# Kernel optimization log

Measured on AMD Instinct MI355X. Metric: run time of the kernel, lower is better.

Reference implementation:

```python
import jax, jax.numpy as jnp
import numpy as np

# Fixed Grossberg constants (registered buffers in the torch module)
TAU = 0.8          # time constant
DECAY = 0.15       # passive decay A
B_CAP = 1.0        # excitatory cap B
C_FLOOR = 0.1      # inhibitory floor C
LAT_INHIB = 3.0    # lateral inhibition strength
DIV_SIGMA = 0.3    # divisive normalization sigma
ALPHA = 1.5        # excitatory gating alpha
BETA = 0.75        # inhibitory gating beta

BATCH = 32768
N = 17
T = 128
DT = 0.05


def _dynamics(state, W_pos, W_neg, feasibility, P):
    """Grossberg shunting ODE right-hand side. state: [B,17]."""
    # valences evaluated with environmental perturbation
    val_eval = state[:, 13:17] + P[:, 13:17]                       # [B,4]
    gate_exc = jax.nn.sigmoid(ALPHA * val_eval)                    # [B,4]
    gate_inh = jax.nn.sigmoid(-BETA * val_eval)                    # [B,4]
    ones9 = jnp.ones_like(state[:, :9])
    ones4 = jnp.ones_like(gate_exc)
    # gates expanded over nodes: only action nodes (9:13) gated
    ge_full = jnp.concatenate([ones9, gate_exc, ones4], axis=1)    # [B,17]
    gi_full = jnp.concatenate([ones9, gate_inh, ones4], axis=1)    # [B,17]
    # row-gating of W is equivalent to gating the matvec output
    exc = ge_full * jnp.einsum('bij,bj->bi', W_pos, state)         # [B,17]
    inh = gi_full * jnp.einsum('bij,bj->bi', W_neg, state)         # [B,17]
    E = jax.nn.relu(exc)
    I = jax.nn.relu(inh)
    # environmental drive routed through shunting terms for need nodes
    E_needs = E[:, :9] + jax.nn.relu(P[:, :9])
    I_needs = I[:, :9] + jax.nn.relu(-P[:, :9])
    # feasibility gates action excitation; selective lateral inhibition:
    # each action inhibited by the (divisively normalized) sum of OTHER actions
    acts = state[:, 9:13]
    other_sum = jnp.sum(acts, axis=1, keepdims=True) - acts
    lateral = LAT_INHIB * other_sum / (DIV_SIGMA + other_sum)
    E_acts = E[:, 9:13] * feasibility
    I_acts = I[:, 9:13] + lateral
    E_full = jnp.concatenate([E_needs, E_acts, E[:, 13:17]], axis=1)
    I_full = jnp.concatenate([I_needs, I_acts, I[:, 13:17]], axis=1)
    # direct additive perturbation only on valence nodes
    P_direct = jnp.concatenate([jnp.zeros_like(state[:, :13]), P[:, 13:17]], axis=1)
    return (-DECAY * state + (B_CAP - state) * E_full
            - (C_FLOOR + state) * I_full + P_direct) / TAU


def setup_inputs() -> dict:
    key = jax.random.key(0)
    k0, k1, k2, k3, k4 = jax.random.split(key, 5)
    state0 = jax.random.uniform(k0, (BATCH, N), dtype=jnp.float32)
    W_pos = 0.2 * jax.random.uniform(k1, (BATCH, N, N), dtype=jnp.float32)
    W_neg = 0.2 * jax.random.uniform(k2, (BATCH, N, N), dtype=jnp.float32)
    feasibility = jax.random.uniform(k3, (BATCH, 4), dtype=jnp.float32)
    perturbation = 0.1 * jax.random.normal(k4, (BATCH, N), dtype=jnp.float32)
    t_eval = jnp.arange(T, dtype=jnp.float32) * DT
    return {"state0": state0, "W_pos": W_pos, "W_neg": W_neg,
            "feasibility": feasibility, "perturbation": perturbation,
            "t_eval": t_eval}


def reference(state0, W_pos, W_neg, feasibility, perturbation, t_eval):
    dt = t_eval[1] - t_eval[0]
    n_steps = t_eval.shape[0] - 1  # static

    def step(s, _):
        ds = _dynamics(s, W_pos, W_neg, feasibility, perturbation)
        raw = s + dt * ds
        new = jnp.concatenate([
            jnp.clip(raw[:, 0:9], 0.0, 1.0),     # needs
            jnp.clip(raw[:, 9:13], 0.0, 1.0),    # actions
            jnp.clip(raw[:, 13:17], -1.0, 1.0),  # valences
        ], axis=1)
        return new, new

    _, traj = jax.lax.scan(step, state0, None, length=n_steps)
    return jnp.concatenate([state0[None], traj], axis=0)  # [T, B, 17]
```

## Files before the change

### kernel.cpp

```cpp
#include <hip/hip_runtime.h>
#include <stdint.h>


typedef _Float16 h2 __attribute__((ext_vector_type(2)));
typedef __fp16 h2raw __attribute__((ext_vector_type(2)));

static constexpr int BATCH = 32768;
static constexpr int NN = 17;
static constexpr int TT = 128;

__device__ __forceinline__ uint32_t pk(float a, float b) {
    h2raw h = __builtin_amdgcn_cvt_pkrtz(a, b);
    return __builtin_bit_cast(uint32_t, h);
}

__device__ __forceinline__ float dot2(uint32_t a, uint32_t b, float c) {
#if __has_builtin(__builtin_amdgcn_fdot2)
    return __builtin_amdgcn_fdot2(__builtin_bit_cast(h2, a),
                                  __builtin_bit_cast(h2, b), c, false);
#else
    h2 ah = __builtin_bit_cast(h2, a), bh = __builtin_bit_cast(h2, b);
    return c + (float)ah.x * (float)bh.x + (float)ah.y * (float)bh.y;
#endif
}

__global__ __launch_bounds__(256, 2) void hotco_kernel(
    const float* __restrict__ state0,
    const float* __restrict__ Wpos,
    const float* __restrict__ Wneg,
    const float* __restrict__ feas,
    const float* __restrict__ P,
    const float* __restrict__ t_eval,
    float* __restrict__ out)
{
    const int tid = blockIdx.x * blockDim.x + threadIdx.x;
    const int lane4 = tid & 3;
    const int b = tid >> 2;
    if (b >= BATCH) return;

    const int base = (lane4 == 0) ? 0 : (4 * lane4 + 1);
    const int nrows = (lane4 == 0) ? 5 : 4;

    constexpr int pA[9] = {0, 2, 4, 5, 7, 9, 11, 13, 15};
    constexpr int pB[9] = {1, 3, -1, 6, 8, 10, 12, 14, 16};

    uint32_t wp[5][9], wn[5][9];
    {
        const float* wpb = Wpos + (size_t)b * (NN * NN);
        const float* wnb = Wneg + (size_t)b * (NN * NN);
#pragma unroll
        for (int t = 0; t < 5; ++t) {
            if (t < nrows) {
                const float* rp = wpb + (base + t) * NN;
                const float* rn = wnb + (base + t) * NN;
#pragma unroll
                for (int c = 0; c < 9; ++c) {
                    float a2 = (pB[c] < 0) ? 0.f : rp[pB[c]];
                    float b2 = (pB[c] < 0) ? 0.f : rn[pB[c]];
                    wp[t][c] = pk(rp[pA[c]], a2);
                    wn[t][c] = pk(rn[pA[c]], b2);
                }
            } else {
#pragma unroll
                for (int c = 0; c < 9; ++c) { wp[t][c] = 0u; wn[t][c] = 0u; }
            }
        }
    }

    uint32_t s2[9];
    {
        float st[17];
#pragma unroll
        for (int j = 0; j < NN; ++j) st[j] = state0[(size_t)b * NN + j];
#pragma unroll
        for (int c = 0; c < 9; ++c)
            s2[c] = pk(st[pA[c]], (pB[c] < 0) ? 0.f : st[pB[c]]);
    }
    float sOwn[5];
#pragma unroll
    for (int t = 0; t < 5; ++t)
        sOwn[t] = (t < nrows) ? state0[(size_t)b * NN + base + t] : 0.f;

    float aE[5], aI[5], pdv[5];
    float gP[4], gF[4];
#pragma unroll
    for (int t = 0; t < 5; ++t) { aE[t] = 0.f; aI[t] = 0.f; pdv[t] = 0.f; }
#pragma unroll
    for (int t = 0; t < 4; ++t) { gP[t] = 0.f; gF[t] = 0.f; }
    if (lane4 < 2) {
#pragma unroll
        for (int t = 0; t < 5; ++t) {
            if (t < nrows) {
                float pv = P[(size_t)b * NN + base + t];
                aE[t] = fmaxf(pv, 0.f);
                aI[t] = fmaxf(-pv, 0.f);
            }
        }
    } else if (lane4 == 2) {
#pragma unroll
        for (int t = 0; t < 4; ++t) {
            gP[t] = P[(size_t)b * NN + 13 + t];
            gF[t] = feas[(size_t)b * 4 + t];
        }
    } else {
#pragma unroll
        for (int t = 0; t < 4; ++t)
            pdv[t] = P[(size_t)b * NN + 13 + t];
    }

    const float lo = (lane4 == 3) ? -1.f : 0.f;
    const float dt = t_eval[1] - t_eval[0];
    const float k1 = dt / 0.8f;
    const float C  = -1.0820212806667226f;

    {
        float* op = out + (size_t)b * NN + base;
#pragma unroll
        for (int t = 0; t < 5; ++t)
            if (t < nrows) op[t] = sOwn[t];
    }
    float* outp = out + (size_t)BATCH * NN + (size_t)b * NN + base;

#pragma unroll 1
    for (int st = 1; st < TT; ++st) {
        float E5[5], I5[5];
#pragma unroll
        for (int t = 0; t < 5; ++t) {
            float ae = 0.f, ai = 0.f;
#pragma unroll
            for (int c = 0; c < 9; ++c) {
                ae = dot2(wp[t][c], s2[c], ae);
                ai = dot2(wn[t][c], s2[c], ai);
            }
            E5[t] = fmaxf(ae, 0.f);
            I5[t] = fmaxf(ai, 0.f);
        }

        if (lane4 == 2) {
            const float sum_acts = sOwn[0] + sOwn[1] + sOwn[2] + sOwn[3];
            h2 q7 = __builtin_bit_cast(h2, s2[7]);
            h2 q8 = __builtin_bit_cast(h2, s2[8]);
            float v13[4] = { (float)q7.x, (float)q7.y, (float)q8.x, (float)q8.y };
#pragma unroll
            for (int t = 0; t < 4; ++t) {
                float v  = v13[t] + gP[t];
                float e1 = __builtin_amdgcn_exp2f(C * v);
                float ge = __builtin_amdgcn_rcpf(fmaf(e1, e1, 1.f));
                float gi = e1 * __builtin_amdgcn_rcpf(1.f + e1);
                E5[t] = ge * E5[t] * gF[t];
                float os  = sum_acts - sOwn[t];
                float lat = fmaf(-0.9f, __builtin_amdgcn_rcpf(0.3f + os), 3.0f);
                I5[t] = fmaf(gi, I5[t], lat);
            }
            E5[4] = 0.f; I5[4] = 0.f;
        } else {
#pragma unroll
            for (int t = 0; t < 5; ++t) { E5[t] += aE[t]; I5[t] += aI[t]; }
        }

#pragma unroll
        for (int t = 0; t < 5; ++t) {
            float s  = sOwn[t];
            float d0 = fmaf(-0.15f, s, pdv[t]);
            float d1 = fmaf(1.f - s, E5[t], d0);
            float d2 = fmaf(-(0.1f + s), I5[t], d1);
            float raw = fmaf(k1, d2, s);
            sOwn[t] = fminf(fmaxf(raw, lo), 1.f);
        }

        uint32_t pk0 = pk(sOwn[0], sOwn[1]);
        uint32_t pk1 = pk(sOwn[2], sOwn[3]);
        uint32_t pk2 = pk(sOwn[4], 0.f);
        s2[0] = (uint32_t)__shfl((int)pk0, 0, 4);
        s2[1] = (uint32_t)__shfl((int)pk1, 0, 4);
        s2[2] = (uint32_t)__shfl((int)pk2, 0, 4);
        s2[3] = (uint32_t)__shfl((int)pk0, 1, 4);
        s2[4] = (uint32_t)__shfl((int)pk1, 1, 4);
        s2[5] = (uint32_t)__shfl((int)pk0, 2, 4);
        s2[6] = (uint32_t)__shfl((int)pk1, 2, 4);
        s2[7] = (uint32_t)__shfl((int)pk0, 3, 4);
        s2[8] = (uint32_t)__shfl((int)pk1, 3, 4);

#pragma unroll
        for (int t = 0; t < 5; ++t)
            if (t < nrows) outp[t] = sOwn[t];
        outp += (size_t)BATCH * NN;
    }
}

extern "C" void kernel_launch(void* const* d_in, const int* in_sizes, int n_in,
                              void* d_out, int out_size, void* d_ws, size_t ws_size,
                              hipStream_t stream) {
    const float* state0 = (const float*)d_in[0];
    const float* Wpos   = (const float*)d_in[1];
    const float* Wneg   = (const float*)d_in[2];
    const float* feasv  = (const float*)d_in[3];
    const float* P      = (const float*)d_in[4];
    const float* t_eval = (const float*)d_in[5];
    float* out = (float*)d_out;

    dim3 grid(BATCH * 4 / 256), block(256);
    hipLaunchKernelGGL(hotco_kernel, grid, block, 0, stream,
                       state0, Wpos, Wneg, feasv, P, t_eval, out);
}
```

Measured before the change: 147.6 us.

## Split excitatory and inhibitory matvecs across separate lanes, use ds_swizzle exchange

Each batch element now uses 8 lanes instead of 4: lanes 0-3 hold W_pos rows and compute the excitatory terms, lanes 4-7 hold W_neg rows and compute the inhibitory terms. The inhibitory results are passed to the excitatory lanes with a ds_swizzle xor-4. The state broadcast now uses ds_swizzle in place of __shfl. This halves per-thread weight registers and dot-product work and lets occupancy bounds rise to 4 waves per SIMD. In exchange it doubles the thread count and adds an extra cross-lane exchange on the serial time-step critical path.

```diff
diff --git a/kernel.cpp b/kernel.cpp
--- a/kernel.cpp
+++ b/kernel.cpp
@@ -13,7 +13,6 @@
     h2raw h = __builtin_amdgcn_cvt_pkrtz(a, b);
     return __builtin_bit_cast(uint32_t, h);
 }
-
 __device__ __forceinline__ float dot2(uint32_t a, uint32_t b, float c) {
 #if __has_builtin(__builtin_amdgcn_fdot2)
     return __builtin_amdgcn_fdot2(__builtin_bit_cast(h2, a),
@@ -23,8 +22,27 @@
     return c + (float)ah.x * (float)bh.x + (float)ah.y * (float)bh.y;
 #endif
 }
-
-__global__ __launch_bounds__(256, 2) void hotco_kernel(
+__device__ __forceinline__ float lo16(uint32_t u) {
+    h2 h = __builtin_bit_cast(h2, u); return (float)h.x;
+}
+__device__ __forceinline__ float hi16(uint32_t u) {
+    h2 h = __builtin_bit_cast(h2, u); return (float)h.y;
+}
+template <int IMM>
+__device__ __forceinline__ uint32_t swz(uint32_t v) {
+    return (uint32_t)__builtin_amdgcn_ds_swizzle((int)v, IMM);
+}
+template <int IMM>
+__device__ __forceinline__ float swzf(float v) {
+    return __builtin_bit_cast(float,
+        (uint32_t)__builtin_amdgcn_ds_swizzle(
+            (int)__builtin_bit_cast(uint32_t, v), IMM));
+}
+
+static constexpr int SWZ_B0 = 0x18, SWZ_B1 = 0x38, SWZ_B2 = 0x58, SWZ_B3 = 0x78;
+static constexpr int SWZ_X4 = 0x101F;
+
+__global__ __launch_bounds__(256, 4) void hotco_kernel(
     const float* __restrict__ state0,
     const float* __restrict__ Wpos,
     const float* __restrict__ Wneg,
@@ -34,35 +52,32 @@
     float* __restrict__ out)
 {
     const int tid = blockIdx.x * blockDim.x + threadIdx.x;
-    const int lane4 = tid & 3;
-    const int b = tid >> 2;
-    if (b >= BATCH) return;
-
-    const int base = (lane4 == 0) ? 0 : (4 * lane4 + 1);
-    const int nrows = (lane4 == 0) ? 5 : 4;
+    const int lq = tid & 7;
+    const int b  = tid >> 3;
+    const int l4 = lq & 3;
+    const bool isE   = lq < 4;
+    const bool isActs = (l4 == 2);
+    const bool isLat  = (lq == 6);
+
+    const int base = (l4 == 0) ? 0 : (4 * l4 + 1);
+    const int nrows = (l4 == 0) ? 5 : 4;
 
     constexpr int pA[9] = {0, 2, 4, 5, 7, 9, 11, 13, 15};
     constexpr int pB[9] = {1, 3, -1, 6, 8, 10, 12, 14, 16};
 
-    uint32_t wp[5][9], wn[5][9];
+    uint32_t w[5][9];
     {
-        const float* wpb = Wpos + (size_t)b * (NN * NN);
-        const float* wnb = Wneg + (size_t)b * (NN * NN);
+        const float* Wb = (isE ? Wpos : Wneg) + (size_t)b * (NN * NN);
 #pragma unroll
         for (int t = 0; t < 5; ++t) {
             if (t < nrows) {
-                const float* rp = wpb + (base + t) * NN;
-                const float* rn = wnb + (base + t) * NN;
-#pragma unroll
-                for (int c = 0; c < 9; ++c) {
-                    float a2 = (pB[c] < 0) ? 0.f : rp[pB[c]];
-                    float b2 = (pB[c] < 0) ? 0.f : rn[pB[c]];
-                    wp[t][c] = pk(rp[pA[c]], a2);
-                    wn[t][c] = pk(rn[pA[c]], b2);
-                }
+                const float* r = Wb + (base + t) * NN;
+#pragma unroll
+                for (int c = 0; c < 9; ++c)
+                    w[t][c] = pk(r[pA[c]], (pB[c] < 0) ? 0.f : r[pB[c]]);
             } else {
 #pragma unroll
-                for (int c = 0; c < 9; ++c) { wp[t][c] = 0u; wn[t][c] = 0u; }
+                for (int c = 0; c < 9; ++c) w[t][c] = 0u;
             }
         }
     }
@@ -81,39 +96,37 @@
     for (int t = 0; t < 5; ++t)
         sOwn[t] = (t < nrows) ? state0[(size_t)b * NN + base + t] : 0.f;
 
-    float aE[5], aI[5], pdv[5];
-    float gP[4], gF[4];
-#pragma unroll
-    for (int t = 0; t < 5; ++t) { aE[t] = 0.f; aI[t] = 0.f; pdv[t] = 0.f; }
-#pragma unroll
-    for (int t = 0; t < 4; ++t) { gP[t] = 0.f; gF[t] = 0.f; }
-    if (lane4 < 2) {
+    float addc[5], pdv[5], gP[4], gm[4];
+#pragma unroll
+    for (int t = 0; t < 5; ++t) { addc[t] = 0.f; pdv[t] = 0.f; }
+#pragma unroll
+    for (int t = 0; t < 4; ++t) { gP[t] = 0.f; gm[t] = 1.f; }
+    if (l4 < 2) {
 #pragma unroll
         for (int t = 0; t < 5; ++t) {
             if (t < nrows) {
                 float pv = P[(size_t)b * NN + base + t];
-                aE[t] = fmaxf(pv, 0.f);
-                aI[t] = fmaxf(-pv, 0.f);
+                addc[t] = isE ? fmaxf(pv, 0.f) : fmaxf(-pv, 0.f);
             }
         }
-    } else if (lane4 == 2) {
+    } else if (isActs) {
 #pragma unroll
         for (int t = 0; t < 4; ++t) {
             gP[t] = P[(size_t)b * NN + 13 + t];
-            gF[t] = feas[(size_t)b * 4 + t];
-        }
-    } else {
+            if (isE) gm[t] = feas[(size_t)b * 4 + t];
+        }
+    } else if (isE) {
 #pragma unroll
         for (int t = 0; t < 4; ++t)
             pdv[t] = P[(size_t)b * NN + 13 + t];
     }
 
-    const float lo = (lane4 == 3) ? -1.f : 0.f;
-    const float dt = t_eval[1] - t_eval[0];
-    const float k1 = dt / 0.8f;
+    const float lo = (l4 == 3) ? -1.f : 0.f;
+    const float dtv = t_eval[1] - t_eval[0];
+    const float k1 = dtv * 1.25f;
     const float C  = -1.0820212806667226f;
 
-    {
+    if (isE) {
         float* op = out + (size_t)b * NN + base;
 #pragma unroll
         for (int t = 0; t < 5; ++t)
@@ -123,67 +136,66 @@
 
 #pragma unroll 1
     for (int st = 1; st < TT; ++st) {
-        float E5[5], I5[5];
-#pragma unroll
-        for (int t = 0; t < 5; ++t) {
-            float ae = 0.f, ai = 0.f;
-#pragma unroll
-            for (int c = 0; c < 9; ++c) {
-                ae = dot2(wp[t][c], s2[c], ae);
-                ai = dot2(wn[t][c], s2[c], ai);
-            }
-            E5[t] = fmaxf(ae, 0.f);
-            I5[t] = fmaxf(ai, 0.f);
-        }
-
-        if (lane4 == 2) {
-            const float sum_acts = sOwn[0] + sOwn[1] + sOwn[2] + sOwn[3];
-            h2 q7 = __builtin_bit_cast(h2, s2[7]);
-            h2 q8 = __builtin_bit_cast(h2, s2[8]);
-            float v13[4] = { (float)q7.x, (float)q7.y, (float)q8.x, (float)q8.y };
+        float R[5];
+#pragma unroll
+        for (int t = 0; t < 5; ++t) {
+            float a = 0.f;
+#pragma unroll
+            for (int c = 0; c < 9; ++c) a = dot2(w[t][c], s2[c], a);
+            R[t] = fmaxf(a, 0.f);
+        }
+
+        float Rp[5];
+        {
+            const float v0 = lo16(s2[7]), v1 = hi16(s2[7]);
+            const float v2 = lo16(s2[8]), v3 = hi16(s2[8]);
+            const float a0 = lo16(s2[5]), a1 = hi16(s2[5]);
+            const float a2 = lo16(s2[6]), a3 = hi16(s2[6]);
+            const float sum_acts = (a0 + a1) + (a2 + a3);
+            const float v13[4] = {v0, v1, v2, v3};
+            const float av[4]  = {a0, a1, a2, a3};
 #pragma unroll
             for (int t = 0; t < 4; ++t) {
                 float v  = v13[t] + gP[t];
                 float e1 = __builtin_amdgcn_exp2f(C * v);
-                float ge = __builtin_amdgcn_rcpf(fmaf(e1, e1, 1.f));
-                float gi = e1 * __builtin_amdgcn_rcpf(1.f + e1);
-                E5[t] = ge * E5[t] * gF[t];
-                float os  = sum_acts - sOwn[t];
+                float t0 = isE ? e1 : 1.0f;
+                float r  = __builtin_amdgcn_rcpf(fmaf(e1, t0, 1.0f));
+                float g  = isE ? r : e1 * r;
+                float gate = isActs ? g * gm[t] : 1.0f;
+                float os  = sum_acts - av[t];
                 float lat = fmaf(-0.9f, __builtin_amdgcn_rcpf(0.3f + os), 3.0f);
-                I5[t] = fmaf(gi, I5[t], lat);
+                float addv = isLat ? lat : addc[t];
+                Rp[t] = fmaf(gate, R[t], addv);
             }
-            E5[4] = 0.f; I5[4] = 0.f;
-        } else {
-#pragma unroll
-            for (int t = 0; t < 5; ++t) { E5[t] += aE[t]; I5[t] += aI[t]; }
-        }
+            Rp[4] = R[4] + addc[4];
+        }
+
+        float Iv[5];
+#pragma unroll
+        for (int t = 0; t < 5; ++t) Iv[t] = swzf<SWZ_X4>(Rp[t]);
 
 #pragma unroll
         for (int t = 0; t < 5; ++t) {
             float s  = sOwn[t];
-            float d0 = fmaf(-0.15f, s, pdv[t]);
-            float d1 = fmaf(1.f - s, E5[t], d0);
-            float d2 = fmaf(-(0.1f + s), I5[t], d1);
-            float raw = fmaf(k1, d2, s);
+            float d  = fmaf(1.f - s, Rp[t], fmaf(-0.15f, s, pdv[t]));
+            d        = fmaf(-(0.1f + s), Iv[t], d);
+            float raw = fmaf(k1, d, s);
             sOwn[t] = fminf(fmaxf(raw, lo), 1.f);
         }
 
-        uint32_t pk0 = pk(sOwn[0], sOwn[1]);
-        uint32_t pk1 = pk(sOwn[2], sOwn[3]);
-        uint32_t pk2 = pk(sOwn[4], 0.f);
-        s2[0] = (uint32_t)__shfl((int)pk0, 0, 4);
-        s2[1] = (uint32_t)__shfl((int)pk1, 0, 4);
-        s2[2] = (uint32_t)__shfl((int)pk2, 0, 4);
-        s2[3] = (uint32_t)__shfl((int)pk0, 1, 4);
-        s2[4] = (uint32_t)__shfl((int)pk1, 1, 4);
-        s2[5] = (uint32_t)__shfl((int)pk0, 2, 4);
-        s2[6] = (uint32_t)__shfl((int)pk1, 2, 4);
-        s2[7] = (uint32_t)__shfl((int)pk0, 3, 4);
-        s2[8] = (uint32_t)__shfl((int)pk1, 3, 4);
-
-#pragma unroll
-        for (int t = 0; t < 5; ++t)
-            if (t < nrows) outp[t] = sOwn[t];
+        uint32_t p0 = pk(sOwn[0], sOwn[1]);
+        uint32_t p1 = pk(sOwn[2], sOwn[3]);
+        uint32_t p2 = pk(sOwn[4], 0.f);
+        s2[0] = swz<SWZ_B0>(p0); s2[1] = swz<SWZ_B0>(p1); s2[2] = swz<SWZ_B0>(p2);
+        s2[3] = swz<SWZ_B1>(p0); s2[4] = swz<SWZ_B1>(p1);
+        s2[5] = swz<SWZ_B2>(p0); s2[6] = swz<SWZ_B2>(p1);
+        s2[7] = swz<SWZ_B3>(p0); s2[8] = swz<SWZ_B3>(p1);
+
+        if (isE) {
+#pragma unroll
+            for (int t = 0; t < 5; ++t)
+                if (t < nrows) outp[t] = sOwn[t];
+        }
         outp += (size_t)BATCH * NN;
     }
 }
@@ -199,7 +211,7 @@
     const float* t_eval = (const float*)d_in[5];
     float* out = (float*)d_out;
 
-    dim3 grid(BATCH * 4 / 256), block(256);
+    dim3 grid(BATCH * 8 / 256), block(256);
     hipLaunchKernelGGL(hotco_kernel, grid, block, 0, stream,
                        state0, Wpos, Wneg, feasv, P, t_eval, out);
 }
```

New measurement: 201.7 us. 1.37x slower.
